# Kernel tuning notes

Hardware: AMD Instinct MI355X
Metric: run time of the kernel (lower is better)

The kernel has to match this reference:

```python
import jax, jax.numpy as jnp
import numpy as np

B, LQ, LF, NW, NFR, E, D, V = 4, 128, 64, 2, 8, 128, 128, 64


def _project(x, W, b):
    # torch Emb_Projection('linear'): Linear then zero-row mask
    y = x @ W + b
    m = 1.0 - jnp.all(y == 0, axis=-1, keepdims=True).astype(y.dtype)
    return y * m


def setup_inputs() -> dict:
    key = jax.random.key(0)
    ks = jax.random.split(key, 12)
    s = lambda k, shape, fan: jax.random.normal(k, shape, jnp.float32) / np.sqrt(fan)
    return {
        "query": jax.random.normal(ks[0], (B, LQ, E), jnp.float32),
        "fragment": jax.random.normal(ks[1], (B, NW, NFR, LF, E), jnp.float32),
        "query_mask": jnp.ones((B, LQ), jnp.float32),
        "fragment_mask": jnp.ones((B, NW, NFR, LF), jnp.float32),
        # learned params (stored [in, out]; torch Linear is x @ W.T with W [out,in])
        "proj_W": s(ks[2], (E, D), E),
        "proj_b": jnp.zeros((D,), jnp.float32),
        "self_att_W": s(ks[3], (NW, D), D),   # n_way Linear(D,1,bias=False)
        "q_att_W": s(ks[4], (D, V), D),
        "f_att_W": s(ks[5], (D, V), D),
        "qf_att_W": s(ks[6], (D, V), D),
        "gate_w": s(ks[7], (V,), V),          # value_gate: Linear(V,1,bias=False)
        "val_w": s(ks[8], (V,), V),           # value_att:  Linear(V,1,bias=False)
    }


def reference(query, fragment, query_mask, fragment_mask, proj_W, proj_b,
              self_att_W, q_att_W, f_att_W, qf_att_W, gate_w, val_w):
    query = _project(query, proj_W, proj_b)          # [B,Lq,D]
    fragment = _project(fragment, proj_W, proj_b)    # [B,NW,NFR,Lf,D]

    # (1) fragment self-attention -> frag_code
    logits = jnp.einsum('bwfld,wd->bwfl', fragment, self_att_W)   # per-way Linear(D,1)
    e = jnp.exp(logits) * fragment_mask
    frag_self_att = e / (e.sum(-1, keepdims=True) + 1e-7)          # [B,NW,NFR,Lf]
    frag_code = (fragment * frag_self_att[..., None]).sum(-2)     # [B,NW,NFR,D]

    # (2) query-to-fragment attention
    frag_r = fragment.reshape(fragment.shape[0], -1, fragment.shape[-2], fragment.shape[-1])  # [B,NF,Lf,D]
    qr = query[:, None]                                            # [B,1,Lq,D]
    q_att = qr @ q_att_W                                           # [B,1,Lq,V]
    f_att = frag_r @ f_att_W                                       # [B,NF,Lf,V]
    # large broadcast product [B,NF,Lf,Lq,D] then project to V
    qf = (qr[:, :, None, :, :] * frag_r[:, :, :, None, :]) @ qf_att_W  # [B,NF,Lf,Lq,V]
    qf = q_att[:, :, None] + f_att[:, :, :, None] + qf
    qf = qf.max(axis=-3)                                           # max over Lf -> [B,NF,Lq,V]

    qf_gate = jax.nn.sigmoid(qf @ gate_w) * query_mask[:, None]    # [B,NF,Lq]
    e2 = jnp.exp(qf @ val_w) * query_mask[:, None]
    qf_norm = e2 / (e2.sum(-1, keepdims=True) + 1e-7)              # [B,NF,Lq]

    query_code = (qr * qf_norm[..., None]).sum(axis=2)             # [B,NF,D]
    query_code = query_code.reshape(frag_code.shape)               # [B,NW,NFR,D]
    return frag_code, query_code, frag_self_att, qf_gate, query
```

## Files before the change

kernel.cpp:

```cpp
#include <hip/hip_runtime.h>
#include <hip/hip_bf16.h>

#define B_   4
#define LQ_  128
#define LF_  64
#define NW_  2
#define NFR_ 8
#define E_   128
#define D_   128
#define V_   64
#define NWF_ (NW_*NFR_)
#define NROW_Q (B_*LQ_)
#define NROW_F (B_*NW_*NFR_*LF_)

using bf16 = __hip_bfloat16;
typedef unsigned short u16;
typedef unsigned int   u32;
typedef __attribute__((ext_vector_type(8))) short  bf16x8;
typedef __attribute__((ext_vector_type(4))) float  f32x4;
typedef __attribute__((ext_vector_type(4))) u32    u32x4;

#define WS_QP    0
#define WS_QATT  65536
#define WS_E2    98304
#define WS_FP16  106496
#define WS_W3T   368640
#define WS_WFT   372736

#define OUT_FRAGCODE  0
#define OUT_QUERYCODE 8192
#define OUT_SELFATT   16384
#define OUT_QFGATE    20480
#define OUT_QUERY     28672

__device__ __forceinline__ float us2f(u16 v) { return __uint_as_float((u32)v << 16); }
__device__ __forceinline__ float lo2f(u32 v) { return __uint_as_float(v << 16); }
__device__ __forceinline__ float hi2f(u32 v) { return __uint_as_float(v & 0xffff0000u); }
__device__ __forceinline__ u16 f2b_raw(float f) {
    u32 u = __float_as_uint(f);
    return (u16)((u + 0x7fffu + ((u >> 16) & 1u)) >> 16);
}
__device__ __forceinline__ u32 pk2(float hi, float lo) {
    return __builtin_amdgcn_perm(__float_as_uint(hi), __float_as_uint(lo), 0x07060302u);
}
template<bool BF> __device__ __forceinline__ float LD(const void* p, int i) {
    return BF ? us2f(((const u16*)p)[i]) : ((const float*)p)[i];
}
template<bool BF> __device__ __forceinline__ void ST(void* p, int i, float v) {
    if (BF) ((u16*)p)[i] = f2b_raw(v); else ((float*)p)[i] = v;
}
template<bool BF> __device__ __forceinline__ u16 LDB(const void* p, int i) {
    return BF ? ((const u16*)p)[i] : f2b_raw(((const float*)p)[i]);
}
__device__ __forceinline__ bool is_bf(const void* qmask) {
    return ((const u16*)qmask)[0] == 0x3F80u;
}

template<bool BF>
__device__ __forceinline__ void proj_body(
    const void* query, const void* fragment, const void* projW, const void* projB,
    const void* qattW, const void* qfW, const void* fattW,
    float* ws, void* out, char* smem)
{
    int bx = blockIdx.x, t = threadIdx.x;
    if (bx >= 72) {
        const void* src = (bx == 72) ? qfW : fattW;
        u16* dst = (u16*)(ws + ((bx == 72) ? WS_W3T : WS_WFT));
        u16* stg = (u16*)smem;
        #pragma unroll
        for (int it = 0; it < 32; ++it) {
            int i = t + 256 * it;
            int k = i >> 6, v = i & 63;
            stg[k * 65 + v] = LDB<BF>(src, i);
        }
        __syncthreads();
        #pragma unroll
        for (int it = 0; it < 32; ++it) {
            int j = t + 256 * it;
            int vo = j >> 7, ko = j & 127;
            dst[vo * 128 + ko] = stg[ko * 65 + vo];
        }
        return;
    }
    u16*   s_x  = (u16*)smem;
    u16*   s_wt = (u16*)(smem + 16384);
    u16*   s_y  = (u16*)(smem + 32768);
    float* s_b  = (float*)(smem + 49152);
    bool isq = (bx < 8);
    int r0 = bx * 64;
    int rowbase = isq ? r0 : (r0 - NROW_Q);
    const void* xsrc = isq ? query : fragment;

    #pragma unroll
    for (int it = 0; it < 16; ++it) {
        int i = t + 256 * it;
        int row = i >> 6, cp = i & 63;
        u32 val;
        if (BF) val = ((const u32*)xsrc)[(size_t)(rowbase + row) * 64 + cp];
        else {
            float2 f = ((const float2*)xsrc)[(size_t)(rowbase + row) * 64 + cp];
            val = ((u32)f2b_raw(f.y) << 16) | f2b_raw(f.x);
        }
        ((u32*)s_x)[row * 64 + (cp ^ ((row & 7) << 2))] = val;
    }
    #pragma unroll
    for (int it = 0; it < 32; ++it) {
        int i = t + 256 * it;
        int k = i >> 6, np = (i & 63) * 2;
        u16 lo, hi;
        if (BF) { u32 v2 = ((const u32*)projW)[i]; lo = (u16)(v2 & 0xffffu); hi = (u16)(v2 >> 16); }
        else { float2 f = ((const float2*)projW)[i]; lo = f2b_raw(f.x); hi = f2b_raw(f.y); }
        s_wt[(np)     * 128 + (k ^ (((np)     & 7) << 3))] = lo;
        s_wt[(np + 1) * 128 + (k ^ (((np + 1) & 7) << 3))] = hi;
    }
    if (t < 128) s_b[t] = LD<BF>(projB, t);
    __syncthreads();

    int lane = t & 63, wave = t >> 6, m = lane & 15, quad = lane >> 4;
    f32x4 acc[8];
    #pragma unroll
    for (int nt = 0; nt < 8; ++nt) { float bv = s_b[nt * 16 + m]; acc[nt] = (f32x4){bv, bv, bv, bv}; }
    int arow = wave * 16 + m;
    int sk = (m & 7) << 3;
    #pragma unroll
    for (int kt = 0; kt < 4; ++kt) {
        int kx = (kt * 32 + quad * 8) ^ sk;
        bf16x8 a = *(const bf16x8*)&s_x[arow * 128 + kx];
        #pragma unroll
        for (int nt = 0; nt < 8; ++nt) {
            bf16x8 b = *(const bf16x8*)&s_wt[(nt * 16 + m) * 128 + kx];
            acc[nt] = __builtin_amdgcn_mfma_f32_16x16x32_bf16(a, b, acc[nt], 0, 0, 0);
        }
    }
    int growbase = r0 + wave * 16 + quad * 4;
    if (!isq) {
        u16* fp16 = (u16*)(ws + WS_FP16);
        #pragma unroll
        for (int nt = 0; nt < 8; ++nt)
            #pragma unroll
            for (int rr = 0; rr < 4; ++rr)
                fp16[(size_t)(growbase + rr - NROW_Q) * 128 + nt * 16 + m] = f2b_raw(acc[nt][rr]);
    } else {
        #pragma unroll
        for (int nt = 0; nt < 8; ++nt)
            #pragma unroll
            for (int rr = 0; rr < 4; ++rr) {
                float v = acc[nt][rr];
                int gr = growbase + rr, col = nt * 16 + m;
                ws[WS_QP + (size_t)gr * 128 + col] = v;
                ST<BF>(out, OUT_QUERY + gr * 128 + col, v);
            }
        __syncthreads();
        #pragma unroll
        for (int nt = 0; nt < 8; ++nt)
            #pragma unroll
            for (int rr = 0; rr < 4; ++rr) {
                int lr = wave * 16 + quad * 4 + rr, col = nt * 16 + m;
                s_y[lr * 128 + (col ^ ((lr & 7) << 3))] = f2b_raw(acc[nt][rr]);
            }
        #pragma unroll
        for (int it = 0; it < 16; ++it) {
            int i = t + 256 * it;
            int k = i >> 5, np = (i & 31) * 2;
            u16 lo, hi;
            if (BF) { u32 v2 = ((const u32*)qattW)[i]; lo = (u16)(v2 & 0xffffu); hi = (u16)(v2 >> 16); }
            else { float2 f = ((const float2*)qattW)[i]; lo = f2b_raw(f.x); hi = f2b_raw(f.y); }
            s_wt[(np)     * 128 + (k ^ (((np)     & 7) << 3))] = lo;
            s_wt[(np + 1) * 128 + (k ^ (((np + 1) & 7) << 3))] = hi;
        }
        __syncthreads();
        f32x4 acc2[4];
        #pragma unroll
        for (int nt = 0; nt < 4; ++nt) acc2[nt] = (f32x4){0.f, 0.f, 0.f, 0.f};
        #pragma unroll
        for (int kt = 0; kt < 4; ++kt) {
            int kx = (kt * 32 + quad * 8) ^ sk;
            bf16x8 a = *(const bf16x8*)&s_y[(wave * 16 + m) * 128 + kx];
            #pragma unroll
            for (int nt = 0; nt < 4; ++nt) {
                bf16x8 b = *(const bf16x8*)&s_wt[(nt * 16 + m) * 128 + kx];
                acc2[nt] = __builtin_amdgcn_mfma_f32_16x16x32_bf16(a, b, acc2[nt], 0, 0, 0);
            }
        }
        #pragma unroll
        for (int nt = 0; nt < 4; ++nt)
            #pragma unroll
            for (int rr = 0; rr < 4; ++rr)
                ws[WS_QATT + (size_t)(growbase + rr) * 64 + nt * 16 + m] = acc2[nt][rr];
    }
}
__global__ __launch_bounds__(256) void k_proj(
    const void* query, const void* fragment, const void* projW, const void* projB,
    const void* qattW, const void* qfW, const void* fattW, const void* qmask,
    float* ws, void* out)
{
    __shared__ char smem[49664];
    if (is_bf(qmask)) proj_body<true >(query, fragment, projW, projB, qattW, qfW, fattW, ws, out, smem);
    else              proj_body<false>(query, fragment, projW, projB, qattW, qfW, fattW, ws, out, smem);
}

template<bool BF>
__device__ __forceinline__ void qf_body(
    const void* saW, const void* fmask, const void* gatew, const void* valw,
    const void* qmask, float* ws, void* out, char* smem)
{
    u16*   s_fp   = (u16*)smem;
    float* s_fatt = (float*)(smem + 16384);
    float* s_pmax = s_fatt;
    float* s_saw  = (float*)(smem + 33792);
    float* s_att  = (float*)(smem + 34304);
    float* s_tmp  = (float*)(smem + 34560);

    int t = threadIdx.x, lane = t & 63, wave = t >> 6;
    int bwf = blockIdx.x >> 3, qt = blockIdx.x & 7;
    int b = bwf >> 4;
    int m = lane & 15, quad = lane >> 4;
    int sk = (m & 7) << 3;

    {
        const u32* src = (const u32*)((const u16*)(ws + WS_FP16)) + (size_t)bwf * 4096;
        u32* d32 = (u32*)s_fp;
        #pragma unroll
        for (int k = 0; k < 16; ++k) {
            int i = t + 256 * k;
            int row = i >> 6, cp = i & 63;
            d32[row * 64 + (cp ^ ((row & 7) << 2))] = src[i];
        }
    }
    const u16* w3t = (const u16*)(ws + WS_W3T);
    const u16* wft = (const u16*)(ws + WS_WFT);
    bf16x8 w3f[4][4], wff[4][4];
    #pragma unroll
    for (int vt = 0; vt < 4; ++vt)
        #pragma unroll
        for (int kt = 0; kt < 4; ++kt) {
            int off = (vt * 16 + m) * 128 + kt * 32 + quad * 8;
            w3f[vt][kt] = *(const bf16x8*)(w3t + off);
            wff[vt][kt] = *(const bf16x8*)(wft + off);
        }
    __syncthreads();

    int lbase = wave * 16;
    {
        bf16x8 afk[4];
        #pragma unroll
        for (int kt = 0; kt < 4; ++kt) {
            int kx = (kt * 32 + quad * 8) ^ sk;
            afk[kt] = *(const bf16x8*)&s_fp[(lbase + m) * 128 + kx];
        }
        #pragma unroll
        for (int vt = 0; vt < 4; ++vt) {
            f32x4 a0 = (f32x4){0.f, 0.f, 0.f, 0.f};
            #pragma unroll
            for (int kt = 0; kt < 4; ++kt)
                a0 = __builtin_amdgcn_mfma_f32_16x16x32_bf16(afk[kt], wff[vt][kt], a0, 0, 0, 0);
            #pragma unroll
            for (int r = 0; r < 4; ++r)
                s_fatt[(lbase + quad * 4 + r) * 68 + vt * 16 + m] = a0[r];
        }
    }
    float qpreg[4][8];
    {
        const float* qprow = ws + WS_QP + (size_t)(b * LQ_ + qt * 16 + m) * 128;
        #pragma unroll
        for (int kt = 0; kt < 4; ++kt) {
            f32x4 x0 = *(const f32x4*)(qprow + kt * 32 + quad * 8);
            f32x4 x1 = *(const f32x4*)(qprow + kt * 32 + quad * 8 + 4);
            qpreg[kt][0] = x0.x; qpreg[kt][1] = x0.y; qpreg[kt][2] = x0.z; qpreg[kt][3] = x0.w;
            qpreg[kt][4] = x1.x; qpreg[kt][5] = x1.y; qpreg[kt][6] = x1.z; qpreg[kt][7] = x1.w;
        }
    }

    float mx[4][4];
    #pragma unroll
    for (int vt = 0; vt < 4; ++vt)
        #pragma unroll
        for (int r = 0; r < 4; ++r) mx[vt][r] = -1e30f;

    #pragma unroll 2
    for (int li = 0; li < 16; ++li) {
        int l = lbase + li;
        bf16x8 af[4];
        #pragma unroll
        for (int kt = 0; kt < 4; ++kt) {
            const u16* p = &s_fp[l * 128 + ((kt * 32 + quad * 8) ^ ((li & 7) << 3))];
            u32x4 fv = *(const u32x4*)p;
            u32x4 av;
            av.x = pk2(qpreg[kt][1] * hi2f(fv.x), qpreg[kt][0] * lo2f(fv.x));
            av.y = pk2(qpreg[kt][3] * hi2f(fv.y), qpreg[kt][2] * lo2f(fv.y));
            av.z = pk2(qpreg[kt][5] * hi2f(fv.z), qpreg[kt][4] * lo2f(fv.z));
            av.w = pk2(qpreg[kt][7] * hi2f(fv.w), qpreg[kt][6] * lo2f(fv.w));
            af[kt] = __builtin_bit_cast(bf16x8, av);
        }
        #pragma unroll
        for (int vt = 0; vt < 4; ++vt) {
            float fa = s_fatt[l * 68 + vt * 16 + m];
            f32x4 acc = (f32x4){fa, fa, fa, fa};
            #pragma unroll
            for (int kt = 0; kt < 4; ++kt)
                acc = __builtin_amdgcn_mfma_f32_16x16x32_bf16(af[kt], w3f[vt][kt], acc, 0, 0, 0);
            #pragma unroll
            for (int r = 0; r < 4; ++r) mx[vt][r] = fmaxf(mx[vt][r], acc[r]);
        }
    }
    #pragma unroll
    for (int vt = 0; vt < 4; ++vt)
        #pragma unroll
        for (int r = 0; r < 4; ++r)
            s_pmax[wave * 1088 + (quad * 4 + r) * 68 + vt * 16 + m] = mx[vt][r];
    __syncthreads();

    {
        int q = t >> 4, vg = t & 15;
        int gq = qt * 16 + q;
        float gp = 0.f, ep = 0.f;
        #pragma unroll
        for (int jj = 0; jj < 4; ++jj) {
            int v = vg * 4 + jj;
            float mval = -1e30f;
            #pragma unroll
            for (int w = 0; w < 4; ++w)
                mval = fmaxf(mval, s_pmax[w * 1088 + q * 68 + v]);
            float qf = mval + ws[WS_QATT + (size_t)(b * LQ_ + gq) * 64 + v];
            gp += qf * LD<BF>(gatew, v);
            ep += qf * LD<BF>(valw, v);
        }
        #pragma unroll
        for (int off = 1; off <= 8; off <<= 1) {
            gp += __shfl_xor(gp, off, 64);
            ep += __shfl_xor(ep, off, 64);
        }
        if (vg == 0) {
            float qm = LD<BF>(qmask, b * LQ_ + gq);
            float g = (1.0f / (1.0f + expf(-gp))) * qm;
            ST<BF>(out, OUT_QFGATE + bwf * LQ_ + gq, g);
            ws[WS_E2 + bwf * LQ_ + gq] = expf(ep) * qm;
        }
    }

    if (qt == 0) {
        if (t < 128) s_saw[t] = LD<BF>(saW, ((bwf >> 3) & 1) * 128 + t);
        __syncthreads();
        int l = t >> 2, j4 = t & 3;
        float p = 0.f;
        #pragma unroll
        for (int it = 0; it < 4; ++it) {
            int koff = j4 * 32 + it * 8;
            const u16* pp = &s_fp[l * 128 + (koff ^ ((l & 7) << 3))];
            u32x4 fv = *(const u32x4*)pp;
            const float* swp = &s_saw[koff];
            p += lo2f(fv.x) * swp[0] + hi2f(fv.x) * swp[1]
               + lo2f(fv.y) * swp[2] + hi2f(fv.y) * swp[3]
               + lo2f(fv.z) * swp[4] + hi2f(fv.z) * swp[5]
               + lo2f(fv.w) * swp[6] + hi2f(fv.w) * swp[7];
        }
        p += __shfl_xor(p, 1, 64);
        p += __shfl_xor(p, 2, 64);
        if (j4 == 0) s_att[l] = expf(p) * LD<BF>(fmask, bwf * LF_ + l);
        __syncthreads();
        if (t < 64) {
            float e = s_att[t], s = e;
            #pragma unroll
            for (int off = 1; off <= 32; off <<= 1) s += __shfl_xor(s, off, 64);
            float nrm = e / (s + 1e-7f);
            s_att[t] = nrm;
            ST<BF>(out, OUT_SELFATT + bwf * LF_ + t, nrm);
        }
        __syncthreads();
        int d = t & 127, half = t >> 7;
        float fc = 0.f;
        #pragma unroll
        for (int li2 = 0; li2 < 32; ++li2) {
            int l2 = half * 32 + li2;
            fc += us2f(s_fp[l2 * 128 + (d ^ ((l2 & 7) << 3))]) * s_att[l2];
        }
        if (half == 1) s_tmp[d] = fc;
        __syncthreads();
        if (half == 0) ST<BF>(out, OUT_FRAGCODE + bwf * D_ + d, fc + s_tmp[d]);
    }
}
__global__ __launch_bounds__(256) void k_qf(
    const void* saW, const void* fmask, const void* gatew, const void* valw,
    const void* qmask, float* ws, void* out)
{
    __shared__ char smem[35072];
    if (is_bf(qmask)) qf_body<true >(saW, fmask, gatew, valw, qmask, ws, out, smem);
    else              qf_body<false>(saW, fmask, gatew, valw, qmask, ws, out, smem);
}

template<bool BF>
__device__ __forceinline__ void qcode_body(const float* ws, void* out,
                                           float* s_n, float* s_part)
{
    int bwf = blockIdx.x, b = bwf >> 4, t = threadIdx.x;
    float e = ws[WS_E2 + bwf * LQ_ + t];
    float s = e;
    #pragma unroll
    for (int off = 1; off <= 32; off <<= 1) s += __shfl_xor(s, off, 64);
    if ((t & 63) == 0) s_part[t >> 6] = s;
    __syncthreads();
    float tot = s_part[0] + s_part[1] + 1e-7f;
    s_n[t] = e / tot;
    __syncthreads();
    float qc = 0.f;
    #pragma unroll 8
    for (int q = 0; q < LQ_; ++q)
        qc += ws[WS_QP + (size_t)(b * LQ_ + q) * 128 + t] * s_n[q];
    ST<BF>(out, OUT_QUERYCODE + bwf * D_ + t, qc);
}
__global__ __launch_bounds__(128) void k_qcode(const void* qmask, const float* ws, void* out)
{
    __shared__ float s_n[LQ_];
    __shared__ float s_part[2];
    if (is_bf(qmask)) qcode_body<true >(ws, out, s_n, s_part);
    else              qcode_body<false>(ws, out, s_n, s_part);
}

extern "C" void kernel_launch(void* const* d_in, const int* in_sizes, int n_in,
                              void* d_out, int out_size, void* d_ws, size_t ws_size,
                              hipStream_t stream)
{
    const void* query    = d_in[0];
    const void* fragment = d_in[1];
    const void* qmask    = d_in[2];
    const void* fmask    = d_in[3];
    const void* projW    = d_in[4];
    const void* projB    = d_in[5];
    const void* saW      = d_in[6];
    const void* qattW    = d_in[7];
    const void* fattW    = d_in[8];
    const void* qfW      = d_in[9];
    const void* gatew    = d_in[10];
    const void* valw     = d_in[11];
    float* ws = (float*)d_ws;

    hipLaunchKernelGGL(k_proj, dim3(74), dim3(256), 0, stream,
                       query, fragment, projW, projB, qattW, qfW, fattW, qmask, ws, d_out);
    hipLaunchKernelGGL(k_qf, dim3(512), dim3(256), 0, stream,
                       saW, fmask, gatew, valw, qmask, ws, d_out);
    hipLaunchKernelGGL(k_qcode, dim3(B_ * NWF_), dim3(128), 0, stream,
                       qmask, ws, d_out);
}
```

Measured before the change: 120.3 us.

## Split weight prep into its own kernel and widen projection and qf parallelism

Weight transposes move into a separate 4-block prep kernel. The projection kernel now runs 288 small blocks of 16 rows that read pre-transposed weights from the workspace, instead of 74 large blocks that staged everything in shared memory. The qf kernel uses 512 threads per block, with waves split across Lf and query halves. It stores f_att and the partial maxima as bf16 in shared memory and prefetches the next fragment row into registers. The aim is better occupancy and less shared-memory traffic, at the cost of an extra kernel launch and reduced precision in the intermediate maxima.

```diff
diff --git a/kernel.cpp b/kernel.cpp
--- a/kernel.cpp
+++ b/kernel.cpp
@@ -26,6 +26,8 @@
 #define WS_FP16  106496
 #define WS_W3T   368640
 #define WS_WFT   372736
+#define WS_PWT   376832
+#define WS_QAT   385024
 
 #define OUT_FRAGCODE  0
 #define OUT_QUERYCODE 8192
@@ -57,146 +59,113 @@
 }
 
 template<bool BF>
+__device__ __forceinline__ void prep_body(const void* src, u16* dst, u16* stg, int N)
+{
+    int t = threadIdx.x;
+    int st = N + 1, total = 128 * N;
+    for (int i = t; i < total; i += 256)
+        stg[(i / N) * st + (i % N)] = LDB<BF>(src, i);
+    __syncthreads();
+    for (int j = t; j < total; j += 256) {
+        int n = j >> 7, k = j & 127;
+        dst[n * 128 + k] = stg[k * st + n];
+    }
+}
+__global__ __launch_bounds__(256) void k_prep(
+    const void* projW, const void* qattW, const void* qfW, const void* fattW,
+    const void* qmask, float* ws)
+{
+    __shared__ u16 stg[128 * 129];
+    int bx = blockIdx.x;
+    const void* src = (bx == 0) ? projW : (bx == 1) ? qattW : (bx == 2) ? qfW : fattW;
+    u16* dst = (u16*)(ws + ((bx == 0) ? WS_PWT : (bx == 1) ? WS_QAT : (bx == 2) ? WS_W3T : WS_WFT));
+    int N = (bx == 0) ? 128 : 64;
+    if (is_bf(qmask)) prep_body<true >(src, dst, stg, N);
+    else              prep_body<false>(src, dst, stg, N);
+}
+
+template<bool BF>
 __device__ __forceinline__ void proj_body(
-    const void* query, const void* fragment, const void* projW, const void* projB,
-    const void* qattW, const void* qfW, const void* fattW,
-    float* ws, void* out, char* smem)
-{
-    int bx = blockIdx.x, t = threadIdx.x;
-    if (bx >= 72) {
-        const void* src = (bx == 72) ? qfW : fattW;
-        u16* dst = (u16*)(ws + ((bx == 72) ? WS_W3T : WS_WFT));
-        u16* stg = (u16*)smem;
-        #pragma unroll
-        for (int it = 0; it < 32; ++it) {
-            int i = t + 256 * it;
-            int k = i >> 6, v = i & 63;
-            stg[k * 65 + v] = LDB<BF>(src, i);
-        }
-        __syncthreads();
-        #pragma unroll
-        for (int it = 0; it < 32; ++it) {
-            int j = t + 256 * it;
-            int vo = j >> 7, ko = j & 127;
-            dst[vo * 128 + ko] = stg[ko * 65 + vo];
-        }
-        return;
-    }
-    u16*   s_x  = (u16*)smem;
-    u16*   s_wt = (u16*)(smem + 16384);
-    u16*   s_y  = (u16*)(smem + 32768);
-    float* s_b  = (float*)(smem + 49152);
-    bool isq = (bx < 8);
-    int r0 = bx * 64;
-    int rowbase = isq ? r0 : (r0 - NROW_Q);
-    const void* xsrc = isq ? query : fragment;
-
-    #pragma unroll
-    for (int it = 0; it < 16; ++it) {
-        int i = t + 256 * it;
-        int row = i >> 6, cp = i & 63;
-        u32 val;
-        if (BF) val = ((const u32*)xsrc)[(size_t)(rowbase + row) * 64 + cp];
+    const void* query, const void* fragment, const void* projB,
+    float* ws, void* out, u16* s_y)
+{
+    int r = blockIdx.x, t = threadIdx.x;
+    int lane = t & 63, wave = t >> 6, m = lane & 15, quad = lane >> 4;
+    bool isq = (r >= 256);
+    int base = isq ? (r - 256) * 16 : r * 16;
+    const void* x = isq ? query : fragment;
+    const u16* pwt = (const u16*)(ws + WS_PWT);
+
+    bf16x8 af[4];
+    #pragma unroll
+    for (int kt = 0; kt < 4; ++kt) {
+        int off = (base + m) * 128 + kt * 32 + quad * 8;
+        if (BF) af[kt] = *(const bf16x8*)((const u16*)x + off);
         else {
-            float2 f = ((const float2*)xsrc)[(size_t)(rowbase + row) * 64 + cp];
-            val = ((u32)f2b_raw(f.y) << 16) | f2b_raw(f.x);
-        }
-        ((u32*)s_x)[row * 64 + (cp ^ ((row & 7) << 2))] = val;
-    }
-    #pragma unroll
-    for (int it = 0; it < 32; ++it) {
-        int i = t + 256 * it;
-        int k = i >> 6, np = (i & 63) * 2;
-        u16 lo, hi;
-        if (BF) { u32 v2 = ((const u32*)projW)[i]; lo = (u16)(v2 & 0xffffu); hi = (u16)(v2 >> 16); }
-        else { float2 f = ((const float2*)projW)[i]; lo = f2b_raw(f.x); hi = f2b_raw(f.y); }
-        s_wt[(np)     * 128 + (k ^ (((np)     & 7) << 3))] = lo;
-        s_wt[(np + 1) * 128 + (k ^ (((np + 1) & 7) << 3))] = hi;
-    }
-    if (t < 128) s_b[t] = LD<BF>(projB, t);
-    __syncthreads();
-
-    int lane = t & 63, wave = t >> 6, m = lane & 15, quad = lane >> 4;
-    f32x4 acc[8];
-    #pragma unroll
-    for (int nt = 0; nt < 8; ++nt) { float bv = s_b[nt * 16 + m]; acc[nt] = (f32x4){bv, bv, bv, bv}; }
-    int arow = wave * 16 + m;
-    int sk = (m & 7) << 3;
-    #pragma unroll
-    for (int kt = 0; kt < 4; ++kt) {
-        int kx = (kt * 32 + quad * 8) ^ sk;
-        bf16x8 a = *(const bf16x8*)&s_x[arow * 128 + kx];
-        #pragma unroll
-        for (int nt = 0; nt < 8; ++nt) {
-            bf16x8 b = *(const bf16x8*)&s_wt[(nt * 16 + m) * 128 + kx];
-            acc[nt] = __builtin_amdgcn_mfma_f32_16x16x32_bf16(a, b, acc[nt], 0, 0, 0);
-        }
-    }
-    int growbase = r0 + wave * 16 + quad * 4;
+            f32x4 a = *(const f32x4*)((const float*)x + off);
+            f32x4 c = *(const f32x4*)((const float*)x + off + 4);
+            u32x4 av;
+            av.x = pk2(a.y, a.x); av.y = pk2(a.w, a.z);
+            av.z = pk2(c.y, c.x); av.w = pk2(c.w, c.z);
+            af[kt] = __builtin_bit_cast(bf16x8, av);
+        }
+    }
+    int nt0 = wave * 2;
+    f32x4 acc[2];
+    #pragma unroll
+    for (int i = 0; i < 2; ++i) {
+        float bv = LD<BF>(projB, (nt0 + i) * 16 + m);
+        acc[i] = (f32x4){bv, bv, bv, bv};
+    }
+    #pragma unroll
+    for (int kt = 0; kt < 4; ++kt)
+        #pragma unroll
+        for (int i = 0; i < 2; ++i) {
+            bf16x8 bfr = *(const bf16x8*)(pwt + ((nt0 + i) * 16 + m) * 128 + kt * 32 + quad * 8);
+            acc[i] = __builtin_amdgcn_mfma_f32_16x16x32_bf16(af[kt], bfr, acc[i], 0, 0, 0);
+        }
     if (!isq) {
         u16* fp16 = (u16*)(ws + WS_FP16);
         #pragma unroll
-        for (int nt = 0; nt < 8; ++nt)
+        for (int i = 0; i < 2; ++i)
             #pragma unroll
             for (int rr = 0; rr < 4; ++rr)
-                fp16[(size_t)(growbase + rr - NROW_Q) * 128 + nt * 16 + m] = f2b_raw(acc[nt][rr]);
+                fp16[(size_t)(base + quad * 4 + rr) * 128 + (nt0 + i) * 16 + m] = f2b_raw(acc[i][rr]);
     } else {
         #pragma unroll
-        for (int nt = 0; nt < 8; ++nt)
+        for (int i = 0; i < 2; ++i)
             #pragma unroll
             for (int rr = 0; rr < 4; ++rr) {
-                float v = acc[nt][rr];
-                int gr = growbase + rr, col = nt * 16 + m;
+                int gr = base + quad * 4 + rr, col = (nt0 + i) * 16 + m;
+                float v = acc[i][rr];
                 ws[WS_QP + (size_t)gr * 128 + col] = v;
                 ST<BF>(out, OUT_QUERY + gr * 128 + col, v);
+                s_y[(quad * 4 + rr) * 132 + col] = f2b_raw(v);
             }
         __syncthreads();
-        #pragma unroll
-        for (int nt = 0; nt < 8; ++nt)
-            #pragma unroll
-            for (int rr = 0; rr < 4; ++rr) {
-                int lr = wave * 16 + quad * 4 + rr, col = nt * 16 + m;
-                s_y[lr * 128 + (col ^ ((lr & 7) << 3))] = f2b_raw(acc[nt][rr]);
-            }
-        #pragma unroll
-        for (int it = 0; it < 16; ++it) {
-            int i = t + 256 * it;
-            int k = i >> 5, np = (i & 31) * 2;
-            u16 lo, hi;
-            if (BF) { u32 v2 = ((const u32*)qattW)[i]; lo = (u16)(v2 & 0xffffu); hi = (u16)(v2 >> 16); }
-            else { float2 f = ((const float2*)qattW)[i]; lo = f2b_raw(f.x); hi = f2b_raw(f.y); }
-            s_wt[(np)     * 128 + (k ^ (((np)     & 7) << 3))] = lo;
-            s_wt[(np + 1) * 128 + (k ^ (((np + 1) & 7) << 3))] = hi;
-        }
-        __syncthreads();
-        f32x4 acc2[4];
-        #pragma unroll
-        for (int nt = 0; nt < 4; ++nt) acc2[nt] = (f32x4){0.f, 0.f, 0.f, 0.f};
+        bf16x8 ay[4];
+        #pragma unroll
+        for (int kt = 0; kt < 4; ++kt)
+            ay[kt] = *(const bf16x8*)&s_y[m * 132 + kt * 32 + quad * 8];
+        const u16* qat = (const u16*)(ws + WS_QAT);
+        f32x4 a2 = (f32x4){0.f, 0.f, 0.f, 0.f};
         #pragma unroll
         for (int kt = 0; kt < 4; ++kt) {
-            int kx = (kt * 32 + quad * 8) ^ sk;
-            bf16x8 a = *(const bf16x8*)&s_y[(wave * 16 + m) * 128 + kx];
-            #pragma unroll
-            for (int nt = 0; nt < 4; ++nt) {
-                bf16x8 b = *(const bf16x8*)&s_wt[(nt * 16 + m) * 128 + kx];
-                acc2[nt] = __builtin_amdgcn_mfma_f32_16x16x32_bf16(a, b, acc2[nt], 0, 0, 0);
-            }
-        }
-        #pragma unroll
-        for (int nt = 0; nt < 4; ++nt)
-            #pragma unroll
-            for (int rr = 0; rr < 4; ++rr)
-                ws[WS_QATT + (size_t)(growbase + rr) * 64 + nt * 16 + m] = acc2[nt][rr];
+            bf16x8 b2 = *(const bf16x8*)(qat + (wave * 16 + m) * 128 + kt * 32 + quad * 8);
+            a2 = __builtin_amdgcn_mfma_f32_16x16x32_bf16(ay[kt], b2, a2, 0, 0, 0);
+        }
+        #pragma unroll
+        for (int rr = 0; rr < 4; ++rr)
+            ws[WS_QATT + (size_t)(base + quad * 4 + rr) * 64 + wave * 16 + m] = a2[rr];
     }
 }
 __global__ __launch_bounds__(256) void k_proj(
-    const void* query, const void* fragment, const void* projW, const void* projB,
-    const void* qattW, const void* qfW, const void* fattW, const void* qmask,
+    const void* query, const void* fragment, const void* projB, const void* qmask,
     float* ws, void* out)
 {
-    __shared__ char smem[49664];
-    if (is_bf(qmask)) proj_body<true >(query, fragment, projW, projB, qattW, qfW, fattW, ws, out, smem);
-    else              proj_body<false>(query, fragment, projW, projB, qattW, qfW, fattW, ws, out, smem);
+    __shared__ u16 s_y[16 * 132];
+    if (is_bf(qmask)) proj_body<true >(query, fragment, projB, ws, out, s_y);
+    else              proj_body<false>(query, fragment, projB, ws, out, s_y);
 }
 
 template<bool BF>
@@ -204,17 +173,17 @@
     const void* saW, const void* fmask, const void* gatew, const void* valw,
     const void* qmask, float* ws, void* out, char* smem)
 {
-    u16*   s_fp   = (u16*)smem;
-    float* s_fatt = (float*)(smem + 16384);
-    float* s_pmax = s_fatt;
-    float* s_saw  = (float*)(smem + 33792);
-    float* s_att  = (float*)(smem + 34304);
-    float* s_tmp  = (float*)(smem + 34560);
+    u16*   s_fp  = (u16*)smem;
+    u16*   s_fa  = (u16*)(smem + 16384);
+    float* s_saw = (float*)(smem + 34816);
+    float* s_att = (float*)(smem + 35328);
+    float* s_tmp = (float*)(smem + 35584);
 
     int t = threadIdx.x, lane = t & 63, wave = t >> 6;
-    int bwf = blockIdx.x >> 3, qt = blockIdx.x & 7;
+    int bwf = blockIdx.x >> 2, qt2 = blockIdx.x & 3;
     int b = bwf >> 4;
     int m = lane & 15, quad = lane >> 4;
+    int lq = wave >> 1, qsub = wave & 1;
     int sk = (m & 7) << 3;
 
     {
@@ -222,46 +191,45 @@
         u32* d32 = (u32*)s_fp;
         #pragma unroll
         for (int k = 0; k < 16; ++k) {
-            int i = t + 256 * k;
+            int i = t + 512 * k;
             int row = i >> 6, cp = i & 63;
             d32[row * 64 + (cp ^ ((row & 7) << 2))] = src[i];
         }
     }
     const u16* w3t = (const u16*)(ws + WS_W3T);
-    const u16* wft = (const u16*)(ws + WS_WFT);
-    bf16x8 w3f[4][4], wff[4][4];
+    bf16x8 w3f[4][4];
     #pragma unroll
     for (int vt = 0; vt < 4; ++vt)
         #pragma unroll
-        for (int kt = 0; kt < 4; ++kt) {
-            int off = (vt * 16 + m) * 128 + kt * 32 + quad * 8;
-            w3f[vt][kt] = *(const bf16x8*)(w3t + off);
-            wff[vt][kt] = *(const bf16x8*)(wft + off);
-        }
-    __syncthreads();
-
-    int lbase = wave * 16;
-    {
+        for (int kt = 0; kt < 4; ++kt)
+            w3f[vt][kt] = *(const bf16x8*)(w3t + (vt * 16 + m) * 128 + kt * 32 + quad * 8);
+    __syncthreads();
+
+    int lbase = lq * 16;
+    if (qsub == 0) {
+        const u16* wft = (const u16*)(ws + WS_WFT);
         bf16x8 afk[4];
         #pragma unroll
-        for (int kt = 0; kt < 4; ++kt) {
-            int kx = (kt * 32 + quad * 8) ^ sk;
-            afk[kt] = *(const bf16x8*)&s_fp[(lbase + m) * 128 + kx];
-        }
+        for (int kt = 0; kt < 4; ++kt)
+            afk[kt] = *(const bf16x8*)&s_fp[(lbase + m) * 128 + ((kt * 32 + quad * 8) ^ sk)];
         #pragma unroll
         for (int vt = 0; vt < 4; ++vt) {
+            bf16x8 wf = *(const bf16x8*)(wft + (vt * 16 + m) * 128 + 0 * 32 + quad * 8);
             f32x4 a0 = (f32x4){0.f, 0.f, 0.f, 0.f};
             #pragma unroll
-            for (int kt = 0; kt < 4; ++kt)
-                a0 = __builtin_amdgcn_mfma_f32_16x16x32_bf16(afk[kt], wff[vt][kt], a0, 0, 0, 0);
+            for (int kt = 0; kt < 4; ++kt) {
+                bf16x8 wk = *(const bf16x8*)(wft + (vt * 16 + m) * 128 + kt * 32 + quad * 8);
+                a0 = __builtin_amdgcn_mfma_f32_16x16x32_bf16(afk[kt], wk, a0, 0, 0, 0);
+                (void)wf;
+            }
             #pragma unroll
             for (int r = 0; r < 4; ++r)
-                s_fatt[(lbase + quad * 4 + r) * 68 + vt * 16 + m] = a0[r];
+                s_fa[(lbase + quad * 4 + r) * 72 + vt * 16 + m] = f2b_raw(a0[r]);
         }
     }
     float qpreg[4][8];
     {
-        const float* qprow = ws + WS_QP + (size_t)(b * LQ_ + qt * 16 + m) * 128;
+        const float* qprow = ws + WS_QP + (size_t)(b * LQ_ + qt2 * 32 + qsub * 16 + m) * 128;
         #pragma unroll
         for (int kt = 0; kt < 4; ++kt) {
             f32x4 x0 = *(const f32x4*)(qprow + kt * 32 + quad * 8);
@@ -270,6 +238,7 @@
             qpreg[kt][4] = x1.x; qpreg[kt][5] = x1.y; qpreg[kt][6] = x1.z; qpreg[kt][7] = x1.w;
         }
     }
+    __syncthreads();
 
     float mx[4][4];
     #pragma unroll
@@ -277,14 +246,23 @@
         #pragma unroll
         for (int r = 0; r < 4; ++r) mx[vt][r] = -1e30f;
 
+    u32x4 fvc[4], fvn[4];
+    #pragma unroll
+    for (int kt = 0; kt < 4; ++kt)
+        fvc[kt] = *(const u32x4*)&s_fp[lbase * 128 + (kt * 32 + quad * 8)];
     #pragma unroll 2
     for (int li = 0; li < 16; ++li) {
+        if (li < 15) {
+            int l2 = lbase + li + 1;
+            #pragma unroll
+            for (int kt = 0; kt < 4; ++kt)
+                fvn[kt] = *(const u32x4*)&s_fp[l2 * 128 + ((kt * 32 + quad * 8) ^ (((li + 1) & 7) << 3))];
+        }
         int l = lbase + li;
         bf16x8 af[4];
         #pragma unroll
         for (int kt = 0; kt < 4; ++kt) {
-            const u16* p = &s_fp[l * 128 + ((kt * 32 + quad * 8) ^ ((li & 7) << 3))];
-            u32x4 fv = *(const u32x4*)p;
+            u32x4 fv = fvc[kt];
             u32x4 av;
             av.x = pk2(qpreg[kt][1] * hi2f(fv.x), qpreg[kt][0] * lo2f(fv.x));
             av.y = pk2(qpreg[kt][3] * hi2f(fv.y), qpreg[kt][2] * lo2f(fv.y));
@@ -294,7 +272,7 @@
         }
         #pragma unroll
         for (int vt = 0; vt < 4; ++vt) {
-            float fa = s_fatt[l * 68 + vt * 16 + m];
+            float fa = us2f(s_fa[l * 72 + vt * 16 + m]);
             f32x4 acc = (f32x4){fa, fa, fa, fa};
             #pragma unroll
             for (int kt = 0; kt < 4; ++kt)
@@ -302,17 +280,20 @@
             #pragma unroll
             for (int r = 0; r < 4; ++r) mx[vt][r] = fmaxf(mx[vt][r], acc[r]);
         }
-    }
+        #pragma unroll
+        for (int kt = 0; kt < 4; ++kt) fvc[kt] = fvn[kt];
+    }
+    __syncthreads();
     #pragma unroll
     for (int vt = 0; vt < 4; ++vt)
         #pragma unroll
         for (int r = 0; r < 4; ++r)
-            s_pmax[wave * 1088 + (quad * 4 + r) * 68 + vt * 16 + m] = mx[vt][r];
+            s_fa[(lq * 32 + qsub * 16 + quad * 4 + r) * 72 + vt * 16 + m] = f2b_raw(mx[vt][r]);
     __syncthreads();
 
     {
         int q = t >> 4, vg = t & 15;
-        int gq = qt * 16 + q;
+        int gq = qt2 * 32 + q;
         float gp = 0.f, ep = 0.f;
         #pragma unroll
         for (int jj = 0; jj < 4; ++jj) {
@@ -320,7 +301,7 @@
             float mval = -1e30f;
             #pragma unroll
             for (int w = 0; w < 4; ++w)
-                mval = fmaxf(mval, s_pmax[w * 1088 + q * 68 + v]);
+                mval = fmaxf(mval, us2f(s_fa[(w * 32 + q) * 72 + v]));
             float qf = mval + ws[WS_QATT + (size_t)(b * LQ_ + gq) * 64 + v];
             gp += qf * LD<BF>(gatew, v);
             ep += qf * LD<BF>(valw, v);
@@ -338,16 +319,16 @@
         }
     }
 
-    if (qt == 0) {
+    if (qt2 == 0) {
         if (t < 128) s_saw[t] = LD<BF>(saW, ((bwf >> 3) & 1) * 128 + t);
         __syncthreads();
-        int l = t >> 2, j4 = t & 3;
+        int l = t >> 3, j8 = t & 7;
+        int swz = (l & 7) << 3;
         float p = 0.f;
         #pragma unroll
-        for (int it = 0; it < 4; ++it) {
-            int koff = j4 * 32 + it * 8;
-            const u16* pp = &s_fp[l * 128 + (koff ^ ((l & 7) << 3))];
-            u32x4 fv = *(const u32x4*)pp;
+        for (int seg = 0; seg < 2; ++seg) {
+            int koff = j8 * 16 + seg * 8;
+            u32x4 fv = *(const u32x4*)&s_fp[l * 128 + (koff ^ swz)];
             const float* swp = &s_saw[koff];
             p += lo2f(fv.x) * swp[0] + hi2f(fv.x) * swp[1]
                + lo2f(fv.y) * swp[2] + hi2f(fv.y) * swp[3]
@@ -356,7 +337,8 @@
         }
         p += __shfl_xor(p, 1, 64);
         p += __shfl_xor(p, 2, 64);
-        if (j4 == 0) s_att[l] = expf(p) * LD<BF>(fmask, bwf * LF_ + l);
+        p += __shfl_xor(p, 4, 64);
+        if (j8 == 0) s_att[l] = expf(p) * LD<BF>(fmask, bwf * LF_ + l);
         __syncthreads();
         if (t < 64) {
             float e = s_att[t], s = e;
@@ -367,23 +349,25 @@
             ST<BF>(out, OUT_SELFATT + bwf * LF_ + t, nrm);
         }
         __syncthreads();
-        int d = t & 127, half = t >> 7;
+        int d = t & 127, grp = t >> 7;
         float fc = 0.f;
         #pragma unroll
-        for (int li2 = 0; li2 < 32; ++li2) {
-            int l2 = half * 32 + li2;
+        for (int li2 = 0; li2 < 16; ++li2) {
+            int l2 = grp * 16 + li2;
             fc += us2f(s_fp[l2 * 128 + (d ^ ((l2 & 7) << 3))]) * s_att[l2];
         }
-        if (half == 1) s_tmp[d] = fc;
+        s_tmp[grp * 128 + d] = fc;
         __syncthreads();
-        if (half == 0) ST<BF>(out, OUT_FRAGCODE + bwf * D_ + d, fc + s_tmp[d]);
-    }
-}
-__global__ __launch_bounds__(256) void k_qf(
+        if (t < 128)
+            ST<BF>(out, OUT_FRAGCODE + bwf * D_ + t,
+                   s_tmp[t] + s_tmp[128 + t] + s_tmp[256 + t] + s_tmp[384 + t]);
+    }
+}
+__global__ __launch_bounds__(512) void k_qf(
     const void* saW, const void* fmask, const void* gatew, const void* valw,
     const void* qmask, float* ws, void* out)
 {
-    __shared__ char smem[35072];
+    __shared__ char smem[37632];
     if (is_bf(qmask)) qf_body<true >(saW, fmask, gatew, valw, qmask, ws, out, smem);
     else              qf_body<false>(saW, fmask, gatew, valw, qmask, ws, out, smem);
 }
@@ -434,9 +418,11 @@
     const void* valw     = d_in[11];
     float* ws = (float*)d_ws;
 
-    hipLaunchKernelGGL(k_proj, dim3(74), dim3(256), 0, stream,
-                       query, fragment, projW, projB, qattW, qfW, fattW, qmask, ws, d_out);
-    hipLaunchKernelGGL(k_qf, dim3(512), dim3(256), 0, stream,
+    hipLaunchKernelGGL(k_prep, dim3(4), dim3(256), 0, stream,
+                       projW, qattW, qfW, fattW, qmask, ws);
+    hipLaunchKernelGGL(k_proj, dim3(288), dim3(256), 0, stream,
+                       query, fragment, projB, qmask, ws, d_out);
+    hipLaunchKernelGGL(k_qf, dim3(256), dim3(512), 0, stream,
                        saW, fmask, gatew, valw, qmask, ws, d_out);
     hipLaunchKernelGGL(k_qcode, dim3(B_ * NWF_), dim3(128), 0, stream,
                        qmask, ws, d_out);
```

After: 114.2 us. -5.1%, faster.
